# Optimization experiments

Hardware: AMD Instinct MI355X
Metric: run time of the kernel (lower is better)

The kernel has to match this reference:

```python
import jax, jax.numpy as jnp
import numpy as np

K, D, SIGMA, SC, EPS = 13, 3, 9.0, 0.1, 1e-5
DEPTH, DIM, HEADS = 6, 256, 8
B, H, W = 1, 48, 64


def _win_start(L, k, d):
    # NATTEN dilated neighborhood window start (static, numpy).
    nb = k // 2
    idx = np.arange(L)
    if d <= 1:
        return np.maximum(idx - nb, 0) + (idx + nb >= L) * (L - idx - nb - 1)
    imodd = idx % d
    a = (L // d) * d
    b = L - a
    right = np.where(imodd < b, L - b + imodd - 2 * nb * d, a + imodd - k * d)
    return np.where(idx - nb * d < 0, imodd,
                    np.where(idx + nb * d >= L, right, idx - nb * d))


def _pb_start(L, k, d):
    # NATTEN relative-position-bias start index (static, numpy).
    nb = k // 2
    idx = np.arange(L)
    if d <= 1:
        return nb + (idx < nb) * (nb - idx) + (idx + nb >= L) * (L - idx - 1 - nb)
    return np.where(idx - nb * d < 0, k - 1 - idx // d,
                    np.where(idx + nb * d >= L, (L - idx - 1) // d, nb))


def _layernorm(x, w, b):
    m = x.mean(-1, keepdims=True)
    v = ((x - m) ** 2).mean(-1, keepdims=True)
    return (x - m) * jax.lax.rsqrt(v + EPS) * w + b


def _ga(x, qkv_w, qkv_b, rpb_l, lr_m_l, proj_w_l, proj_b_l):
    # x: (B,H,W,C) -> neighborhood attention with RPB + learned gaussian mask.
    b, h, w, c = x.shape
    hd = c // HEADS
    scale = hd ** -0.5
    qkv = (x @ qkv_w.T + qkv_b).reshape(b, h, w, 3, HEADS, hd)
    qkv = jnp.transpose(qkv, (3, 0, 4, 1, 2, 5))  # (3,B,n,H,W,d)
    q, k, v = qkv[0] * scale, qkv[1], qkv[2]
    sh, sw = _win_start(h, K, D), _win_start(w, K, D)
    ph, pw = _pb_start(h, K, D), _pb_start(w, K, D)
    taps = np.arange(K)
    ih = sh[:, None] + D * taps  # (H,K) key rows per query row
    iw = sw[:, None] + D * taps  # (W,K)
    kg = k[:, :, ih][:, :, :, :, iw]  # (B,n,H,K,W,K,d)
    vg = v[:, :, ih][:, :, :, :, iw]
    attn = jnp.einsum('bnhwd,bnhiwjd->bnhwij', q, kg)  # (B,n,H,W,K,K)
    bi = ph[:, None] + taps
    bj = pw[:, None] + taps
    bias = rpb_l[:, bi][:, :, :, bj]  # (n,H,K,W,K)
    attn = attn + jnp.transpose(bias, (0, 1, 3, 2, 4))[None]
    crd = jnp.arange(K, dtype=x.dtype)
    g = jnp.exp(-((crd[None, :] - K // 2) ** 2 + (crd[:, None] - K // 2) ** 2)
                / (2.0 * SIGMA ** 2))
    ker = g + lr_m_l / SC  # (K,K)
    attn = attn * ker[None, None, None, None]
    attn = jax.nn.softmax(attn.reshape(b, HEADS, h, w, K * K), axis=-1)
    attn = attn.reshape(b, HEADS, h, w, K, K)
    out = jnp.einsum('bnhwij,bnhiwjd->bnhwd', attn, vg)
    out = jnp.transpose(out, (0, 2, 3, 1, 4)).reshape(b, h, w, c)
    return out @ proj_w_l.T + proj_b_l


def setup_inputs() -> dict:
    key = jax.random.key(0)
    ks = jax.random.split(key, 8)
    s = 0.02
    return {
        'x': jax.random.normal(ks[0], (B, DIM, H, W), jnp.float32),
        'ln1_w': jnp.ones((DEPTH, DIM), jnp.float32),
        'ln1_b': jnp.zeros((DEPTH, DIM), jnp.float32),
        'qkv_w': jax.random.normal(ks[1], (DEPTH, 3 * DIM, DIM), jnp.float32) * s,
        'qkv_b': jnp.zeros((DEPTH, 3 * DIM), jnp.float32),
        'rpb': jax.random.normal(ks[2], (DEPTH, HEADS, 2 * K - 1, 2 * K - 1), jnp.float32) * s,
        'lr_m': jnp.ones((DEPTH, K, K), jnp.float32) * (SC * 0.5),
        'proj_w': jax.random.normal(ks[3], (DEPTH, DIM, DIM), jnp.float32) * s,
        'proj_b': jnp.zeros((DEPTH, DIM), jnp.float32),
        'ln2_w': jnp.ones((DEPTH, DIM), jnp.float32),
        'ln2_b': jnp.zeros((DEPTH, DIM), jnp.float32),
        'fc1_w': jax.random.normal(ks[4], (DEPTH, 4 * DIM, DIM), jnp.float32) * s,
        'fc1_b': jnp.zeros((DEPTH, 4 * DIM), jnp.float32),
        'fc2_w': jax.random.normal(ks[5], (DEPTH, DIM, 4 * DIM), jnp.float32) * s,
        'fc2_b': jnp.zeros((DEPTH, DIM), jnp.float32),
        'normf_w': jnp.ones((DIM,), jnp.float32),
        'normf_b': jnp.zeros((DIM,), jnp.float32),
    }


def reference(x, ln1_w, ln1_b, qkv_w, qkv_b, rpb, lr_m, proj_w, proj_b,
              ln2_w, ln2_b, fc1_w, fc1_b, fc2_w, fc2_b, normf_w, normf_b):
    b, c, h, w = x.shape
    t = jnp.transpose(x, (0, 2, 3, 1)).reshape(b, h * w, c)
    for l in range(ln1_w.shape[0]):
        shortcut = t
        y = _layernorm(t, ln1_w[l], ln1_b[l]).reshape(b, h, w, c)
        y = _ga(y, qkv_w[l], qkv_b[l], rpb[l], lr_m[l], proj_w[l], proj_b[l])
        t = shortcut + y.reshape(b, h * w, c)
        m = _layernorm(t, ln2_w[l], ln2_b[l])
        m = jax.nn.gelu(m @ fc1_w[l].T + fc1_b[l], approximate=False)
        m = m @ fc2_w[l].T + fc2_b[l]
        t = t + m
    t = _layernorm(t, normf_w, normf_b)
    return jnp.transpose(t.reshape(b, h, w, c), (0, 3, 1, 2))
```

## Files before the change

### kernel.cpp

```cpp
#include <hip/hip_runtime.h>
#include <hip/hip_bf16.h>
#include <math.h>

#define DIMC   256
#define HH     48
#define WW     64
#define MROWS  (HH*WW)
#define NHEADS 8
#define HD     32
#define KTAP   13
#define NTAPS  (KTAP*KTAP)
#define DIL    3
#define NB     6
#define EPSLN  1e-5f
#define QSCALE 0.17677669529663687f

typedef __attribute__((ext_vector_type(8))) short bf16x8;
typedef __attribute__((ext_vector_type(4))) float f32x4;
typedef _Float16 __f16;
typedef __f16 f16x2 __attribute__((ext_vector_type(2)));

__device__ __forceinline__ f16x2 pkh(float a, float b) {
    auto r = __builtin_amdgcn_cvt_pkrtz(a, b);
    return __builtin_bit_cast(f16x2, r);
}
__device__ __forceinline__ f16x2 bch(unsigned u) {
    return __builtin_bit_cast(f16x2, u);
}

__device__ __forceinline__ int win_start(int i, int L) {
    int imodd = i % DIL;
    if (i - NB * DIL < 0) return imodd;
    if (i + NB * DIL >= L) {
        int a = (L / DIL) * DIL;
        int b = L - a;
        if (imodd < b) return L - b + imodd - 2 * NB * DIL;
        return a + imodd - KTAP * DIL;
    }
    return i - NB * DIL;
}
__device__ __forceinline__ int pb_start(int i, int L) {
    if (i - NB * DIL < 0) return KTAP - 1 - i / DIL;
    if (i + NB * DIL >= L) return (L - 1 - i) / DIL;
    return NB;
}

__global__ __launch_bounds__(256) void cvt_all_kernel(const float* __restrict__ w0,
                                                      const float* __restrict__ w1,
                                                      const float* __restrict__ w2,
                                                      const float* __restrict__ w3,
                                                      __hip_bfloat16* __restrict__ o0,
                                                      __hip_bfloat16* __restrict__ o1,
                                                      __hip_bfloat16* __restrict__ o2,
                                                      __hip_bfloat16* __restrict__ o3) {
    int i = blockIdx.x * 256 + threadIdx.x;
    const float* in;
    __hip_bfloat16* out;
    int off;
    if (i < 294912)      { in = w0; out = o0; off = i; }
    else if (i < 393216) { in = w1; out = o1; off = i - 294912; }
    else if (i < 786432) { in = w2; out = o2; off = i - 393216; }
    else                 { in = w3; out = o3; off = i - 786432; }
    float4 v = ((const float4*)in)[off];
    union { __hip_bfloat16 h[4]; ushort4 u; } p;
    p.h[0] = __float2bfloat16(v.x);
    p.h[1] = __float2bfloat16(v.y);
    p.h[2] = __float2bfloat16(v.z);
    p.h[3] = __float2bfloat16(v.w);
    ((ushort4*)out)[off] = p.u;
}

__global__ void transpose_in_kernel(const float* __restrict__ x, float* __restrict__ t) {
    int m = blockIdx.x;
    int c = threadIdx.x;
    t[m * DIMC + c] = x[c * MROWS + m];
}

template <typename OutT, int TRANS>
__global__ __launch_bounds__(256) void ln_kernel(const float* __restrict__ in,
                                                 const float* __restrict__ w,
                                                 const float* __restrict__ b,
                                                 OutT* __restrict__ out) {
    __shared__ float s1[4], s2[4];
    int m = blockIdx.x;
    int c = threadIdx.x;
    float v = in[m * DIMC + c];
    float a = v, q = v * v;
    #pragma unroll
    for (int o = 32; o > 0; o >>= 1) {
        a += __shfl_xor(a, o);
        q += __shfl_xor(q, o);
    }
    if ((threadIdx.x & 63) == 0) { s1[threadIdx.x >> 6] = a; s2[threadIdx.x >> 6] = q; }
    __syncthreads();
    float mean = (s1[0] + s1[1] + s1[2] + s1[3]) * (1.0f / DIMC);
    float var  = (s2[0] + s2[1] + s2[2] + s2[3]) * (1.0f / DIMC) - mean * mean;
    float r = (v - mean) * rsqrtf(var + EPSLN) * w[c] + b[c];
    if (TRANS) {
        out[c * MROWS + m] = (OutT)r;
    } else {
        if constexpr (sizeof(OutT) == 2) out[m * DIMC + c] = __float2bfloat16(r);
        else                             out[m * DIMC + c] = r;
    }
}

#define LDP 72
template <int EPI, typename OutT>
__global__ __launch_bounds__(256) void gemm_mfma_kernel(const __hip_bfloat16* __restrict__ A,
                                                        const __hip_bfloat16* __restrict__ Wt,
                                                        const float* __restrict__ bias,
                                                        const float* __restrict__ res,
                                                        OutT* __restrict__ C,
                                                        int M, int N, int K) {
    __shared__ __hip_bfloat16 As[64][LDP];
    __shared__ __hip_bfloat16 Ws[64][LDP];
    int tid = threadIdx.x;
    int bm = blockIdx.y * 64, bn = blockIdx.x * 64;
    int lane = tid & 63, wid = tid >> 6;
    int wr = wid >> 1, wc = wid & 1;
    int fr = lane & 15, fq = lane >> 4;
    f32x4 acc[2][2] = {};

    for (int k0 = 0; k0 < K; k0 += 64) {
        #pragma unroll
        for (int i = 0; i < 4; i++) {
            int idx = tid + i * 256;
            int r = idx >> 4, c = (idx & 15) << 2;
            *(uint2*)&As[r][c] = *(const uint2*)&A[(size_t)(bm + r) * K + k0 + c];
            *(uint2*)&Ws[r][c] = *(const uint2*)&Wt[(size_t)(bn + r) * K + k0 + c];
        }
        __syncthreads();
        #pragma unroll
        for (int kk = 0; kk < 2; kk++) {
            int kb = kk * 32 + fq * 8;
            bf16x8 af[2], bfr[2];
            #pragma unroll
            for (int i = 0; i < 2; i++) {
                union { uint4 u; bf16x8 v; } ua, ub;
                ua.u = *(const uint4*)&As[wr * 32 + i * 16 + fr][kb];
                af[i] = ua.v;
                ub.u = *(const uint4*)&Ws[wc * 32 + i * 16 + fr][kb];
                bfr[i] = ub.v;
            }
            #pragma unroll
            for (int i = 0; i < 2; i++)
                #pragma unroll
                for (int j = 0; j < 2; j++)
                    acc[i][j] = __builtin_amdgcn_mfma_f32_16x16x32_bf16(
                        af[i], bfr[j], acc[i][j], 0, 0, 0);
        }
        __syncthreads();
    }
    #pragma unroll
    for (int i = 0; i < 2; i++) {
        int mbase = bm + wr * 32 + i * 16 + fq * 4;
        #pragma unroll
        for (int j = 0; j < 2; j++) {
            int n = bn + wc * 32 + j * 16 + fr;
            float bv = bias[n];
            #pragma unroll
            for (int r = 0; r < 4; r++) {
                int m = mbase + r;
                float v = acc[i][j][r] + bv;
                if (EPI == 1) v = v * 0.5f * (1.0f + erff(v * 0.70710678118654752f));
                if (EPI == 2) v += res[(size_t)m * N + n];
                if constexpr (sizeof(OutT) == 2) C[(size_t)m * N + n] = __float2bfloat16(v);
                else                             C[(size_t)m * N + n] = v;
            }
        }
    }
}

__global__ __launch_bounds__(512, 4) void attn_kernel(const float* __restrict__ qkv,
                                                      const float* __restrict__ rpb,
                                                      const float* __restrict__ lrm,
                                                      __hip_bfloat16* __restrict__ out) {
    __shared__ __align__(16) unsigned KVd[KTAP * WW * 20];
    __shared__ float rpbs[625];
    __shared__ float kers[NTAPS];

    int tid = threadIdx.x;
    int h = blockIdx.x >> 3;
    int n = blockIdx.x & 7;
    int q = tid >> 3;
    int c = tid & 7;
    int shh = win_start(h, HH);
    int ph  = pb_start(h, HH);
    int sww = win_start(q, WW);
    int pwq = pb_start(q, WW);
    int mrow = h * WW + q;

    for (int i = tid; i < 625; i += 512) rpbs[i] = rpb[n * 625 + i];
    if (tid < NTAPS) {
        int ti = tid / KTAP, tj = tid - KTAP * ti;
        float dx = (float)(tj - NB), dy = (float)(ti - NB);
        kers[tid] = __expf(-(dx * dx + dy * dy) * (1.0f / 162.0f)) + lrm[tid] * 10.0f;
    }

    float4 kreg[14], qv[8];
    #pragma unroll
    for (int it = 0; it < 7; ++it) {
        int tau = tid + 512 * it;
        if (tau < 3328) {
            int row = tau >> 2, j = tau & 3;
            int ti0 = row >> 6, col = row & 63;
            int ihr = shh + DIL * ti0;
            const float4* g = (const float4*)(qkv + (size_t)(ihr * WW + col) * 768
                                              + DIMC + n * HD + 8 * j);
            kreg[2 * it] = g[0]; kreg[2 * it + 1] = g[1];
        }
    }
    {
        const float4* qg = (const float4*)(qkv + (size_t)mrow * 768 + n * HD);
        #pragma unroll
        for (int i = 0; i < 8; ++i) qv[i] = qg[i];
    }

    #pragma unroll
    for (int it = 0; it < 7; ++it) {
        int tau = tid + 512 * it;
        if (tau < 3328) {
            int row = tau >> 2, j = tau & 3;
            float4 u0 = kreg[2 * it], u1 = kreg[2 * it + 1];
            uint4 w;
            w.x = __builtin_bit_cast(unsigned, pkh(u0.x, u0.y));
            w.y = __builtin_bit_cast(unsigned, pkh(u0.z, u0.w));
            w.z = __builtin_bit_cast(unsigned, pkh(u1.x, u1.y));
            w.w = __builtin_bit_cast(unsigned, pkh(u1.z, u1.w));
            *(uint4*)&KVd[row * 20 + j * 4] = w;
        }
    }
    f16x2 qh[16];
    #pragma unroll
    for (int i = 0; i < 8; ++i) {
        qh[2 * i]     = pkh(qv[i].x * QSCALE, qv[i].y * QSCALE);
        qh[2 * i + 1] = pkh(qv[i].z * QSCALE, qv[i].w * QSCALE);
    }
    __syncthreads();

    float4 vA[6];
    #pragma unroll
    for (int it = 0; it < 3; ++it) {
        int tau = tid + 512 * it;
        int row = tau >> 2, j = tau & 3;
        int ti0 = row >> 6, col = row & 63;
        int ihr = shh + DIL * ti0;
        const float4* g = (const float4*)(qkv + (size_t)(ihr * WW + col) * 768
                                          + 2 * DIMC + n * HD + 8 * j);
        vA[2 * it] = g[0]; vA[2 * it + 1] = g[1];
    }

    float p[22];
    float smax = -1e30f;
    {
        int ti = 0, tj = c, tt = c;
        int row = sww + 3 * c;
        #pragma unroll
        for (int k = 0; k < 22; ++k) {
            if (tt < NTAPS) {
                const unsigned* kp = KVd + row * 20;
                uint4 r0 = *(const uint4*)(kp);
                uint4 r1 = *(const uint4*)(kp + 4);
                uint4 r2 = *(const uint4*)(kp + 8);
                uint4 r3 = *(const uint4*)(kp + 12);
                f16x2 sa = {}, sb = {}, sc2 = {}, sd = {};
                sa  += qh[0]  * bch(r0.x); sb  += qh[1]  * bch(r0.y);
                sc2 += qh[2]  * bch(r0.z); sd  += qh[3]  * bch(r0.w);
                sa  += qh[4]  * bch(r1.x); sb  += qh[5]  * bch(r1.y);
                sc2 += qh[6]  * bch(r1.z); sd  += qh[7]  * bch(r1.w);
                sa  += qh[8]  * bch(r2.x); sb  += qh[9]  * bch(r2.y);
                sc2 += qh[10] * bch(r2.z); sd  += qh[11] * bch(r2.w);
                sa  += qh[12] * bch(r3.x); sb  += qh[13] * bch(r3.y);
                sc2 += qh[14] * bch(r3.z); sd  += qh[15] * bch(r3.w);
                f16x2 st = (sa + sb) + (sc2 + sd);
                float s = (float)st.x + (float)st.y;
                s += rpbs[(ph + ti) * 25 + pwq + tj];
                s *= kers[tt];
                p[k] = s;
                smax = fmaxf(smax, s);
            } else {
                p[k] = -1e30f;
            }
            tj += 8; row += 24;
            if (tj >= KTAP) { tj -= KTAP; ++ti; row += 25; }
            tt += 8;
        }
    }
    __syncthreads();

    #pragma unroll
    for (int it = 0; it < 3; ++it) {
        int tau = tid + 512 * it;
        int row = tau >> 2, j = tau & 3;
        float4 u0 = vA[2 * it], u1 = vA[2 * it + 1];
        uint4 w;
        w.x = __builtin_bit_cast(unsigned, pkh(u0.x, u0.y));
        w.y = __builtin_bit_cast(unsigned, pkh(u0.z, u0.w));
        w.z = __builtin_bit_cast(unsigned, pkh(u1.x, u1.y));
        w.w = __builtin_bit_cast(unsigned, pkh(u1.z, u1.w));
        *(uint4*)&KVd[row * 20 + j * 4] = w;
    }
    float4 vB[8];
    #pragma unroll
    for (int it = 3; it < 7; ++it) {
        int tau = tid + 512 * it;
        if (tau < 3328) {
            int row = tau >> 2, j = tau & 3;
            int ti0 = row >> 6, col = row & 63;
            int ihr = shh + DIL * ti0;
            const float4* g = (const float4*)(qkv + (size_t)(ihr * WW + col) * 768
                                              + 2 * DIMC + n * HD + 8 * j);
            vB[2 * (it - 3)] = g[0]; vB[2 * (it - 3) + 1] = g[1];
        }
    }

    #pragma unroll
    for (int o = 1; o < 8; o <<= 1) smax = fmaxf(smax, __shfl_xor(smax, o));
    float ssum = 0.0f;
    #pragma unroll
    for (int k = 0; k < 22; ++k) {
        float e = __expf(p[k] - smax);
        p[k] = e;
        ssum += e;
    }
    #pragma unroll
    for (int o = 1; o < 8; o <<= 1) ssum += __shfl_xor(ssum, o);
    float inv = 1.0f / ssum;
    #pragma unroll
    for (int k = 0; k < 22; ++k) p[k] *= inv;

    #pragma unroll
    for (int it = 3; it < 7; ++it) {
        int tau = tid + 512 * it;
        if (tau < 3328) {
            int row = tau >> 2, j = tau & 3;
            float4 u0 = vB[2 * (it - 3)], u1 = vB[2 * (it - 3) + 1];
            uint4 w;
            w.x = __builtin_bit_cast(unsigned, pkh(u0.x, u0.y));
            w.y = __builtin_bit_cast(unsigned, pkh(u0.z, u0.w));
            w.z = __builtin_bit_cast(unsigned, pkh(u1.x, u1.y));
            w.w = __builtin_bit_cast(unsigned, pkh(u1.z, u1.w));
            *(uint4*)&KVd[row * 20 + j * 4] = w;
        }
    }
    __syncthreads();

    f16x2 acc2[16] = {};
    {
        int ti = 0, tj = c, tt = c;
        int row = sww + 3 * c;
        #pragma unroll
        for (int k = 0; k < 22; ++k) {
            if (tt < NTAPS) {
                const unsigned* vp = KVd + row * 20;
                uint4 r0 = *(const uint4*)(vp);
                uint4 r1 = *(const uint4*)(vp + 4);
                uint4 r2 = *(const uint4*)(vp + 8);
                uint4 r3 = *(const uint4*)(vp + 12);
                f16x2 p2 = pkh(p[k], p[k]);
                acc2[0]  += p2 * bch(r0.x); acc2[1]  += p2 * bch(r0.y);
                acc2[2]  += p2 * bch(r0.z); acc2[3]  += p2 * bch(r0.w);
                acc2[4]  += p2 * bch(r1.x); acc2[5]  += p2 * bch(r1.y);
                acc2[6]  += p2 * bch(r1.z); acc2[7]  += p2 * bch(r1.w);
                acc2[8]  += p2 * bch(r2.x); acc2[9]  += p2 * bch(r2.y);
                acc2[10] += p2 * bch(r2.z); acc2[11] += p2 * bch(r2.w);
                acc2[12] += p2 * bch(r3.x); acc2[13] += p2 * bch(r3.y);
                acc2[14] += p2 * bch(r3.z); acc2[15] += p2 * bch(r3.w);
            }
            tj += 8; row += 24;
            if (tj >= KTAP) { tj -= KTAP; ++ti; row += 25; }
            tt += 8;
        }
    }
    f16x2 r8v[8];
    {
        bool b = (c & 4);
        #pragma unroll
        for (int i = 0; i < 8; ++i) {
            f16x2 keep = b ? acc2[i + 8] : acc2[i];
            f16x2 send = b ? acc2[i] : acc2[i + 8];
            float sf = __shfl_xor(__builtin_bit_cast(float, send), 4);
            r8v[i] = keep + __builtin_bit_cast(f16x2, sf);
        }
    }
    f16x2 r4v[4];
    {
        bool b = (c & 2);
        #pragma unroll
        for (int i = 0; i < 4; ++i) {
            f16x2 keep = b ? r8v[i + 4] : r8v[i];
            f16x2 send = b ? r8v[i] : r8v[i + 4];
            float sf = __shfl_xor(__builtin_bit_cast(float, send), 2);
            r4v[i] = keep + __builtin_bit_cast(f16x2, sf);
        }
    }
    f16x2 r2v[2];
    {
        bool b = (c & 1);
        #pragma unroll
        for (int i = 0; i < 2; ++i) {
            f16x2 keep = b ? r4v[i + 2] : r4v[i];
            f16x2 send = b ? r4v[i] : r4v[i + 2];
            float sf = __shfl_xor(__builtin_bit_cast(float, send), 1);
            r2v[i] = keep + __builtin_bit_cast(f16x2, sf);
        }
    }
    union { __hip_bfloat16 hh[4]; ushort4 u4; } ow;
    ow.hh[0] = __float2bfloat16((float)r2v[0].x);
    ow.hh[1] = __float2bfloat16((float)r2v[0].y);
    ow.hh[2] = __float2bfloat16((float)r2v[1].x);
    ow.hh[3] = __float2bfloat16((float)r2v[1].y);
    *(ushort4*)&out[(size_t)mrow * DIMC + n * HD + c * 4] = ow.u4;
}

extern "C" void kernel_launch(void* const* d_in, const int* in_sizes, int n_in,
                              void* d_out, int out_size, void* d_ws, size_t ws_size,
                              hipStream_t stream) {
    const float* x      = (const float*)d_in[0];
    const float* ln1_w  = (const float*)d_in[1];
    const float* ln1_b  = (const float*)d_in[2];
    const float* qkv_w  = (const float*)d_in[3];
    const float* qkv_b  = (const float*)d_in[4];
    const float* rpb    = (const float*)d_in[5];
    const float* lr_m   = (const float*)d_in[6];
    const float* proj_w = (const float*)d_in[7];
    const float* proj_b = (const float*)d_in[8];
    const float* ln2_w  = (const float*)d_in[9];
    const float* ln2_b  = (const float*)d_in[10];
    const float* fc1_w  = (const float*)d_in[11];
    const float* fc1_b  = (const float*)d_in[12];
    const float* fc2_w  = (const float*)d_in[13];
    const float* fc2_b  = (const float*)d_in[14];
    const float* nf_w   = (const float*)d_in[15];
    const float* nf_b   = (const float*)d_in[16];
    float* out = (float*)d_out;

    char* ws = (char*)d_ws;
    float*          t        = (float*)ws;
    float*          qkvb     = (float*)(ws + 3145728);
    __hip_bfloat16* y        = (__hip_bfloat16*)(ws + 12582912);
    __hip_bfloat16* attn_out = (__hip_bfloat16*)(ws + 14155776);
    __hip_bfloat16* m1       = (__hip_bfloat16*)(ws + 15728640);
    __hip_bfloat16* qkv_wb   = (__hip_bfloat16*)(ws + 22020096);
    __hip_bfloat16* proj_wb  = (__hip_bfloat16*)(ws + 24379392);
    __hip_bfloat16* fc1_wb   = (__hip_bfloat16*)(ws + 25165824);
    __hip_bfloat16* fc2_wb   = (__hip_bfloat16*)(ws + 28311552);

    cvt_all_kernel<<<1179648 / 256, 256, 0, stream>>>(
        qkv_w, proj_w, fc1_w, fc2_w, qkv_wb, proj_wb, fc1_wb, fc2_wb);

    transpose_in_kernel<<<MROWS, 256, 0, stream>>>(x, t);

    for (int l = 0; l < 6; l++) {
        const __hip_bfloat16* qw  = qkv_wb  + (size_t)l * 768 * 256;
        const __hip_bfloat16* pw  = proj_wb + (size_t)l * 256 * 256;
        const __hip_bfloat16* f1w = fc1_wb  + (size_t)l * 1024 * 256;
        const __hip_bfloat16* f2w = fc2_wb  + (size_t)l * 256 * 1024;
        const float* qb  = qkv_b  + (size_t)l * 768;
        const float* pb  = proj_b + (size_t)l * 256;
        const float* f1b = fc1_b  + (size_t)l * 1024;
        const float* f2b = fc2_b  + (size_t)l * 256;
        const float* rp  = rpb    + (size_t)l * NHEADS * 25 * 25;
        const float* lm  = lr_m   + (size_t)l * NTAPS;

        ln_kernel<__hip_bfloat16, 0><<<MROWS, 256, 0, stream>>>(
            t, ln1_w + l * 256, ln1_b + l * 256, y);
        gemm_mfma_kernel<0, float><<<dim3(768 / 64, MROWS / 64), 256, 0, stream>>>(
            y, qw, qb, nullptr, qkvb, MROWS, 768, 256);
        attn_kernel<<<HH * NHEADS, 512, 0, stream>>>(qkvb, rp, lm, attn_out);
        gemm_mfma_kernel<2, float><<<dim3(256 / 64, MROWS / 64), 256, 0, stream>>>(
            attn_out, pw, pb, t, t, MROWS, 256, 256);
        ln_kernel<__hip_bfloat16, 0><<<MROWS, 256, 0, stream>>>(
            t, ln2_w + l * 256, ln2_b + l * 256, y);
        gemm_mfma_kernel<1, __hip_bfloat16><<<dim3(1024 / 64, MROWS / 64), 256, 0, stream>>>(
            y, f1w, f1b, nullptr, m1, MROWS, 1024, 256);
        gemm_mfma_kernel<2, float><<<dim3(256 / 64, MROWS / 64), 256, 0, stream>>>(
            m1, f2w, f2b, t, t, MROWS, 256, 1024);
    }

    ln_kernel<float, 1><<<MROWS, 256, 0, stream>>>(t, nf_w, nf_b, out);
}
```

Before: 418.2 us.

## Use 1024-thread GEMM blocks with register prefetch; raise attention wave priority

The GEMM moves from 256 to 1024 threads per 64x64 tile. Each wave now owns a single 16x16 MFMA output, and each thread stages one uint2 of A and W per k-step. The next k-tile's global loads are prefetched into registers while the current tile is computed, overlapping memory latency with MFMA work. The attention kernel also wraps its two inner dot-product loops in s_setprio to favour those waves. The trade-off is that each wave does less work per LDS read, so fragment reuse is lower, and synchronisation across 16 waves per block costs more.

```diff
diff --git a/kernel.cpp b/kernel.cpp
--- a/kernel.cpp
+++ b/kernel.cpp
@@ -106,68 +106,55 @@
 
 #define LDP 72
 template <int EPI, typename OutT>
-__global__ __launch_bounds__(256) void gemm_mfma_kernel(const __hip_bfloat16* __restrict__ A,
-                                                        const __hip_bfloat16* __restrict__ Wt,
-                                                        const float* __restrict__ bias,
-                                                        const float* __restrict__ res,
-                                                        OutT* __restrict__ C,
-                                                        int M, int N, int K) {
+__global__ __launch_bounds__(1024) void gemm_mfma_kernel(const __hip_bfloat16* __restrict__ A,
+                                                         const __hip_bfloat16* __restrict__ Wt,
+                                                         const float* __restrict__ bias,
+                                                         const float* __restrict__ res,
+                                                         OutT* __restrict__ C,
+                                                         int M, int N, int K) {
     __shared__ __hip_bfloat16 As[64][LDP];
     __shared__ __hip_bfloat16 Ws[64][LDP];
     int tid = threadIdx.x;
     int bm = blockIdx.y * 64, bn = blockIdx.x * 64;
     int lane = tid & 63, wid = tid >> 6;
-    int wr = wid >> 1, wc = wid & 1;
+    int wr = wid & 3, wc = wid >> 2;
     int fr = lane & 15, fq = lane >> 4;
-    f32x4 acc[2][2] = {};
+    int sr = tid >> 4, sc = (tid & 15) << 2;
+    f32x4 acc = {};
+
+    uint2 ra, rw;
+    ra = *(const uint2*)&A[(size_t)(bm + sr) * K + sc];
+    rw = *(const uint2*)&Wt[(size_t)(bn + sr) * K + sc];
 
     for (int k0 = 0; k0 < K; k0 += 64) {
-        #pragma unroll
-        for (int i = 0; i < 4; i++) {
-            int idx = tid + i * 256;
-            int r = idx >> 4, c = (idx & 15) << 2;
-            *(uint2*)&As[r][c] = *(const uint2*)&A[(size_t)(bm + r) * K + k0 + c];
-            *(uint2*)&Ws[r][c] = *(const uint2*)&Wt[(size_t)(bn + r) * K + k0 + c];
-        }
+        *(uint2*)&As[sr][sc] = ra;
+        *(uint2*)&Ws[sr][sc] = rw;
         __syncthreads();
+        if (k0 + 64 < K) {
+            ra = *(const uint2*)&A[(size_t)(bm + sr) * K + k0 + 64 + sc];
+            rw = *(const uint2*)&Wt[(size_t)(bn + sr) * K + k0 + 64 + sc];
+        }
         #pragma unroll
         for (int kk = 0; kk < 2; kk++) {
             int kb = kk * 32 + fq * 8;
-            bf16x8 af[2], bfr[2];
-            #pragma unroll
-            for (int i = 0; i < 2; i++) {
-                union { uint4 u; bf16x8 v; } ua, ub;
-                ua.u = *(const uint4*)&As[wr * 32 + i * 16 + fr][kb];
-                af[i] = ua.v;
-                ub.u = *(const uint4*)&Ws[wc * 32 + i * 16 + fr][kb];
-                bfr[i] = ub.v;
-            }
-            #pragma unroll
-            for (int i = 0; i < 2; i++)
-                #pragma unroll
-                for (int j = 0; j < 2; j++)
-                    acc[i][j] = __builtin_amdgcn_mfma_f32_16x16x32_bf16(
-                        af[i], bfr[j], acc[i][j], 0, 0, 0);
+            union { uint4 u; bf16x8 v; } ua, ub;
+            ua.u = *(const uint4*)&As[wr * 16 + fr][kb];
+            ub.u = *(const uint4*)&Ws[wc * 16 + fr][kb];
+            acc = __builtin_amdgcn_mfma_f32_16x16x32_bf16(ua.v, ub.v, acc, 0, 0, 0);
         }
         __syncthreads();
     }
-    #pragma unroll
-    for (int i = 0; i < 2; i++) {
-        int mbase = bm + wr * 32 + i * 16 + fq * 4;
-        #pragma unroll
-        for (int j = 0; j < 2; j++) {
-            int n = bn + wc * 32 + j * 16 + fr;
-            float bv = bias[n];
-            #pragma unroll
-            for (int r = 0; r < 4; r++) {
-                int m = mbase + r;
-                float v = acc[i][j][r] + bv;
-                if (EPI == 1) v = v * 0.5f * (1.0f + erff(v * 0.70710678118654752f));
-                if (EPI == 2) v += res[(size_t)m * N + n];
-                if constexpr (sizeof(OutT) == 2) C[(size_t)m * N + n] = __float2bfloat16(v);
-                else                             C[(size_t)m * N + n] = v;
-            }
-        }
+    int mbase = bm + wr * 16 + fq * 4;
+    int n = bn + wc * 16 + fr;
+    float bv = bias[n];
+    #pragma unroll
+    for (int r = 0; r < 4; r++) {
+        int m = mbase + r;
+        float v = acc[r] + bv;
+        if (EPI == 1) v = v * 0.5f * (1.0f + erff(v * 0.70710678118654752f));
+        if (EPI == 2) v += res[(size_t)m * N + n];
+        if constexpr (sizeof(OutT) == 2) C[(size_t)m * N + n] = __float2bfloat16(v);
+        else                             C[(size_t)m * N + n] = v;
     }
 }
 
@@ -252,6 +239,7 @@
 
     float p[22];
     float smax = -1e30f;
+    __builtin_amdgcn_s_setprio(1);
     {
         int ti = 0, tj = c, tt = c;
         int row = sww + 3 * c;
@@ -286,6 +274,7 @@
             tt += 8;
         }
     }
+    __builtin_amdgcn_s_setprio(0);
     __syncthreads();
 
     #pragma unroll
@@ -346,6 +335,7 @@
     __syncthreads();
 
     f16x2 acc2[16] = {};
+    __builtin_amdgcn_s_setprio(1);
     {
         int ti = 0, tj = c, tt = c;
         int row = sww + 3 * c;
@@ -372,6 +362,7 @@
             tt += 8;
         }
     }
+    __builtin_amdgcn_s_setprio(0);
     f16x2 r8v[8];
     {
         bool b = (c & 4);
@@ -465,16 +456,16 @@
 
         ln_kernel<__hip_bfloat16, 0><<<MROWS, 256, 0, stream>>>(
             t, ln1_w + l * 256, ln1_b + l * 256, y);
-        gemm_mfma_kernel<0, float><<<dim3(768 / 64, MROWS / 64), 256, 0, stream>>>(
+        gemm_mfma_kernel<0, float><<<dim3(768 / 64, MROWS / 64), 1024, 0, stream>>>(
             y, qw, qb, nullptr, qkvb, MROWS, 768, 256);
         attn_kernel<<<HH * NHEADS, 512, 0, stream>>>(qkvb, rp, lm, attn_out);
-        gemm_mfma_kernel<2, float><<<dim3(256 / 64, MROWS / 64), 256, 0, stream>>>(
+        gemm_mfma_kernel<2, float><<<dim3(256 / 64, MROWS / 64), 1024, 0, stream>>>(
             attn_out, pw, pb, t, t, MROWS, 256, 256);
         ln_kernel<__hip_bfloat16, 0><<<MROWS, 256, 0, stream>>>(
             t, ln2_w + l * 256, ln2_b + l * 256, y);
-        gemm_mfma_kernel<1, __hip_bfloat16><<<dim3(1024 / 64, MROWS / 64), 256, 0, stream>>>(
+        gemm_mfma_kernel<1, __hip_bfloat16><<<dim3(1024 / 64, MROWS / 64), 1024, 0, stream>>>(
             y, f1w, f1b, nullptr, m1, MROWS, 1024, 256);
-        gemm_mfma_kernel<2, float><<<dim3(256 / 64, MROWS / 64), 256, 0, stream>>>(
+        gemm_mfma_kernel<2, float><<<dim3(256 / 64, MROWS / 64), 1024, 0, stream>>>(
             m1, f2w, f2b, t, t, MROWS, 256, 1024);
     }
 
```

New measurement: 404.7 us. 1.03x faster.
